# Kernel tuning notes

Measured on AMD Instinct MI355X. Metric: run time of the kernel, lower is better.

Reference implementation:

```python
import jax, jax.numpy as jnp
import numpy as np
from jax import lax


def _causal_depthwise_conv(x, conv_w, conv_b):
    # x: [B, L, D]; conv_w: [D, 1, K]; conv_b: [D]
    K = conv_w.shape[-1]
    xc = jnp.transpose(x, (0, 2, 1))                      # [B, D, L]
    xc = jnp.pad(xc, ((0, 0), (0, 0), (K - 1, 0)))        # left (causal) pad
    D = xc.shape[1]
    y = lax.conv_general_dilated(
        xc, conv_w, window_strides=(1,), padding='VALID',
        dimension_numbers=('NCH', 'OIH', 'NCH'), feature_group_count=D)
    y = y + conv_b[None, :, None]
    return jnp.transpose(y, (0, 2, 1))                    # [B, L, D]


def setup_inputs() -> dict:
    key = jax.random.key(0)
    ks = jax.random.split(key, 7)
    B, L, Dm, S, K = 4, 4096, 2048, 512, 4
    s = 0.02
    x = jax.random.normal(ks[0], (B, L, Dm), dtype=jnp.float32)
    Wxproj = jax.random.normal(ks[1], (2 * S + 1, Dm), dtype=jnp.float32) * s
    Winproj = jax.random.normal(ks[2], (S, Dm), dtype=jnp.float32) * s
    Woutproj = jax.random.normal(ks[3], (Dm, S), dtype=jnp.float32) * s
    conv_w = jax.random.normal(ks[4], (Dm, 1, K), dtype=jnp.float32) * 0.5
    conv_b = jax.random.normal(ks[5], (Dm,), dtype=jnp.float32) * 0.02
    A_log = jnp.log(jnp.arange(1, S + 1, dtype=jnp.float32))
    D = jnp.ones((Dm,), dtype=jnp.float32)
    return {"x": x, "Wxproj": Wxproj, "Winproj": Winproj, "Woutproj": Woutproj,
            "conv_w": conv_w, "conv_b": conv_b, "A_log": A_log, "D": D}


def reference(x, Wxproj, Winproj, Woutproj, conv_w, conv_b, A_log, D):
    S = A_log.shape[0]
    # causal depthwise conv (Conv1d with padding=K-1, truncated to seq_len)
    x_conv = _causal_depthwise_conv(x, conv_w, conv_b)     # [B, L, Dm]
    # SSM parameters from raw x (matches original: x_proj applied to x, not x_conv)
    ssm_params = jnp.einsum('bld,pd->blp', x, Wxproj)      # [B, L, 2S+1]
    Bmat = ssm_params[..., :S]
    Cmat = ssm_params[..., S:2 * S]
    delta = jax.nn.softplus(ssm_params[..., 2 * S:])       # [B, L, 1]
    A = -jnp.exp(A_log)                                    # [S]
    deltaA = jnp.exp(A[None, None, :] * delta)             # [B, L, S]
    x_state = jnp.einsum('bld,sd->bls', x_conv, Winproj)   # [B, L, S]
    Bu = delta * Bmat * x_state                            # [B, L, S]
    # h_t = deltaA_t * h_{t-1} + Bu_t  via associative scan
    def combine(c1, c2):
        a1, b1 = c1
        a2, b2 = c2
        return a1 * a2, a2 * b1 + b2
    _, h = lax.associative_scan(combine, (deltaA, Bu), axis=1)  # [B, L, S]
    h_mod = Cmat * h
    out = jnp.einsum('bls,ds->bld', h_mod, Woutproj) + D[None, None, :] * x_conv
    return out
```

## Files before the change

kernel.cpp:

```cpp
#include <hip/hip_runtime.h>
#include <math.h>

typedef __bf16 bf16_t;
typedef __bf16 bf16x8 __attribute__((ext_vector_type(8)));
typedef __bf16 bf16x4 __attribute__((ext_vector_type(4)));
typedef float  f32x4  __attribute__((ext_vector_type(4)));
typedef float  f32x16 __attribute__((ext_vector_type(16)));

constexpr int Bb  = 4;
constexpr int L   = 4096;
constexpr int Dm  = 2048;
constexpr int S   = 512;
constexpr int M   = Bb * L;
constexpr int NP  = 2 * S + 1;
constexpr int PST = 1024;
constexpr int CL  = 128;
constexpr int NCH = L / CL;
constexpr int TL  = 32;
constexpr int NTC = L / TL;

#define AS1 __attribute__((address_space(1)))
#define AS3 __attribute__((address_space(3)))

__global__ __launch_bounds__(256)
void f2b_kernel(const float* __restrict__ in, bf16_t* __restrict__ out,
                long out8, long in_elems)
{
    long i = (long)blockIdx.x * 256 + threadIdx.x;
    if (i >= out8) return;
    long e = i * 8;
    bf16x8 o;
    if (e + 8 <= in_elems) {
        float4 v0 = *(const float4*)(in + e);
        float4 v1 = *(const float4*)(in + e + 4);
        o[0] = (bf16_t)v0.x; o[1] = (bf16_t)v0.y;
        o[2] = (bf16_t)v0.z; o[3] = (bf16_t)v0.w;
        o[4] = (bf16_t)v1.x; o[5] = (bf16_t)v1.y;
        o[6] = (bf16_t)v1.z; o[7] = (bf16_t)v1.w;
    } else {
        #pragma unroll
        for (int k = 0; k < 8; ++k)
            o[k] = (e + k < in_elems) ? (bf16_t)in[e + k] : (bf16_t)0.f;
    }
    *(bf16x8*)(out + e) = o;
}

__global__ __launch_bounds__(256)
void conv_fused8(const float* __restrict__ x, const float* __restrict__ w,
                 const float* __restrict__ bias,
                 bf16_t* __restrict__ xcb, bf16_t* __restrict__ xb)
{
    const float4* x4 = (const float4*)x;
    int g    = blockIdx.x * 256 + threadIdx.x;
    int d8   = g & 255;
    int rest = g >> 8;
    int c    = rest & (NTC - 1);
    int b    = rest >> 7;
    int d    = d8 * 8;

    float wv[8][4];
    #pragma unroll
    for (int j = 0; j < 8; ++j)
        *(float4*)wv[j] = *(const float4*)&w[(d + j) * 4];
    float bsv[8];
    *(float4*)&bsv[0] = *(const float4*)&bias[d];
    *(float4*)&bsv[4] = *(const float4*)&bias[d + 4];

    const int l0 = c * TL;
    const size_t rowbase = (size_t)b * L;

    float win[3][8];
    #pragma unroll
    for (int i = 0; i < 3; ++i) {
        int lp = l0 - 3 + i;
        if (lp >= 0) {
            size_t rb4 = (rowbase + lp) * 512 + d8 * 2;
            *(float4*)&win[i][0] = x4[rb4];
            *(float4*)&win[i][4] = x4[rb4 + 1];
        } else {
            #pragma unroll
            for (int j = 0; j < 8; ++j) win[i][j] = 0.f;
        }
    }

    for (int t = 0; t < TL; ++t) {
        size_t m = rowbase + l0 + t;
        size_t rb4 = m * 512 + d8 * 2;
        float cur[8];
        *(float4*)&cur[0] = x4[rb4];
        *(float4*)&cur[4] = x4[rb4 + 1];

        bf16x8 oc, ox;
        #pragma unroll
        for (int j = 0; j < 8; ++j) {
            float a = bsv[j];
            a = fmaf(win[0][j], wv[j][0], a);
            a = fmaf(win[1][j], wv[j][1], a);
            a = fmaf(win[2][j], wv[j][2], a);
            a = fmaf(cur[j],    wv[j][3], a);
            oc[j] = (bf16_t)a;
            ox[j] = (bf16_t)cur[j];
        }
        *(bf16x8*)(xcb + m * Dm + d) = oc;
        *(bf16x8*)(xb  + m * Dm + d) = ox;

        #pragma unroll
        for (int j = 0; j < 8; ++j) {
            win[0][j] = win[1][j]; win[1][j] = win[2][j]; win[2][j] = cur[j];
        }
    }
}

__global__ __launch_bounds__(256)
void gemv_delta(const bf16_t* __restrict__ x_bf, const bf16_t* __restrict__ wdt,
                float* __restrict__ delta)
{
    int m    = blockIdx.x * 4 + (threadIdx.x >> 6);
    int lane = threadIdx.x & 63;
    const bf16x8* xr = (const bf16x8*)(x_bf + (size_t)m * Dm);
    const bf16x8* wr = (const bf16x8*)wdt;
    float s = 0.f;
    #pragma unroll
    for (int i = 0; i < 4; ++i) {
        bf16x8 a = xr[i * 64 + lane];
        bf16x8 b = wr[i * 64 + lane];
        #pragma unroll
        for (int j = 0; j < 8; ++j) s += (float)a[j] * (float)b[j];
    }
    #pragma unroll
    for (int off = 32; off >= 1; off >>= 1) s += __shfl_xor(s, off, 64);
    if (lane == 0) {
        delta[m] = (s > 20.f) ? s : log1pf(__expf(s));
    }
}

__device__ __forceinline__ void stage_slabA(const bf16_t* __restrict__ A,
    bf16_t* lds, int ldsbase, int row0, int K, int kcol, int mh,
    int wid, int lrow, int cswz)
{
    #pragma unroll
    for (int round = 0; round < 2; ++round) {
        int Rb = round * 128 + mh * 64 + wid * 8;
        const bf16_t* src = A + (size_t)(row0 + Rb + lrow) * K + kcol + cswz;
        __builtin_amdgcn_global_load_lds(
            (AS1 void*)src, (AS3 void*)(lds + ldsbase + Rb * 64), 16, 0, 0);
    }
}

__device__ __forceinline__ void stage_slabA128(const bf16_t* __restrict__ A,
    bf16_t* lds, int ldsbase, int row0, int K, int kcol,
    int wid, int lrow, int cswz)
{
    #pragma unroll
    for (int round = 0; round < 2; ++round) {
        int Rb = round * 64 + wid * 8;
        const bf16_t* src = A + (size_t)(row0 + Rb + lrow) * K + kcol + cswz;
        __builtin_amdgcn_global_load_lds(
            (AS1 void*)src, (AS3 void*)(lds + ldsbase + Rb * 64), 16, 0, 0);
    }
}

__device__ __forceinline__ void stage_slabB(const bf16_t* __restrict__ B,
    bf16_t* lds, int ldsbase, int col0, int K, int kcol, int nh,
    int wid, int lrow, int cswz)
{
    #pragma unroll
    for (int round = 0; round < 2; ++round) {
        int c  = round * 8 + wid;
        int Rb = (c >> 2) * 64 + nh * 32 + (c & 3) * 8;
        const bf16_t* src = B + (size_t)(col0 + Rb + lrow) * K + kcol + cswz;
        __builtin_amdgcn_global_load_lds(
            (AS1 void*)src, (AS3 void*)(lds + ldsbase + Rb * 64), 16, 0, 0);
    }
}

template <int MH>
__device__ __forceinline__ void load_fragsA32(const bf16_t* lds, int Abase,
    int wm, int l31, int kh, bf16x8 (&af)[2][4])
{
    #pragma unroll
    for (int mi2 = 0; mi2 < 2; ++mi2) {
        const int R = wm * 128 + (MH * 2 + mi2) * 32 + l31;
        #pragma unroll
        for (int ks = 0; ks < 4; ++ks)
            af[mi2][ks] = *(const bf16x8*)(lds + Abase + R * 64 +
                            ((ks * 16 + kh * 8) ^ ((R & 7) << 3)));
    }
}

template <int MI>
__device__ __forceinline__ void load_fragsA32h(const bf16_t* lds, int Abase,
    int wm, int l31, int kh, bf16x8 (&af)[4])
{
    const int R = wm * 64 + MI * 32 + l31;
    #pragma unroll
    for (int ks = 0; ks < 4; ++ks)
        af[ks] = *(const bf16x8*)(lds + Abase + R * 64 +
                    ((ks * 16 + kh * 8) ^ ((R & 7) << 3)));
}

template <int NH>
__device__ __forceinline__ void load_fragsB32(const bf16_t* lds, int Bbase,
    int wn, int l31, int kh, bf16x8 (&bfr)[4])
{
    const int R = wn * 64 + NH * 32 + l31;
    #pragma unroll
    for (int ks = 0; ks < 4; ++ks)
        bfr[ks] = *(const bf16x8*)(lds + Bbase + R * 64 +
                    ((ks * 16 + kh * 8) ^ ((R & 7) << 3)));
}

template <int MH, int NH>
__device__ __forceinline__ void do_mfma32(bf16x8 (&af)[2][4], bf16x8 (&bfr)[4],
                                          f32x16 (&acc)[4][2])
{
    __builtin_amdgcn_s_setprio(1);
    #pragma unroll
    for (int ks = 0; ks < 4; ++ks)
        #pragma unroll
        for (int mi2 = 0; mi2 < 2; ++mi2)
            acc[MH * 2 + mi2][NH] = __builtin_amdgcn_mfma_f32_32x32x16_bf16(
                af[mi2][ks], bfr[ks], acc[MH * 2 + mi2][NH], 0, 0, 0);
    __builtin_amdgcn_s_setprio(0);
}

template <int MI, int NJ>
__device__ __forceinline__ void do_mfma32h(bf16x8 (&af)[4], bf16x8 (&bfr)[4],
                                           f32x16 (&acc)[2][2])
{
    __builtin_amdgcn_s_setprio(1);
    #pragma unroll
    for (int ks = 0; ks < 4; ++ks)
        acc[MI][NJ] = __builtin_amdgcn_mfma_f32_32x32x16_bf16(
            af[ks], bfr[ks], acc[MI][NJ], 0, 0, 0);
    __builtin_amdgcn_s_setprio(0);
}

#define WAITBAR(N) do { \
    asm volatile("s_waitcnt vmcnt(" #N ")" ::: "memory"); \
    __builtin_amdgcn_s_barrier(); } while (0)

template <int EPI>
__global__ __launch_bounds__(512, 2)
void gemm8p(const bf16_t* __restrict__ A, const bf16_t* __restrict__ B,
            int N, int K, int NT,
            bf16_t* __restrict__ Cb, float* __restrict__ Cf,
            const float* __restrict__ e0, const bf16_t* __restrict__ eb)
{
    extern __shared__ __align__(16) char smem_raw[];
    bf16_t* lds = (bf16_t*)smem_raw;

    const int tid  = threadIdx.x;
    const int lane = tid & 63;
    const int wid  = tid >> 6;
    const int wm   = wid >> 2;
    const int wn   = wid & 3;
    const int l31  = lane & 31;
    const int kh   = lane >> 5;
    const int row0 = blockIdx.x * 256;
    const int col0 = blockIdx.y * 256;
    const int lrow = lane >> 3;
    const int cswz = 8 * ((lane & 7) ^ lrow);

    f32x16 acc[4][2];
    #pragma unroll
    for (int i = 0; i < 4; ++i)
        #pragma unroll
        for (int j = 0; j < 2; ++j)
            #pragma unroll
            for (int g = 0; g < 16; ++g) acc[i][j][g] = 0.f;

    stage_slabA(A, lds, 0,     row0, K, 0, 0, wid, lrow, cswz);
    stage_slabB(B, lds, 16384, col0, K, 0, 0, wid, lrow, cswz);
    stage_slabB(B, lds, 16384, col0, K, 0, 1, wid, lrow, cswz);
    stage_slabA(A, lds, 0,     row0, K, 0, 1, wid, lrow, cswz);

    for (int kt = 0; kt < NT; ++kt) {
        const int cur = kt & 1, nxt = cur ^ 1;
        const int Abase = cur * 32768, Bbase = cur * 32768 + 16384;
        const int An = nxt * 32768,   Bn = nxt * 32768 + 16384;
        const int kc = (kt + 1 < NT ? kt + 1 : kt) * 64;

        bf16x8 af[2][4], bfr[4];

        WAITBAR(4);
        load_fragsA32<0>(lds, Abase, wm, l31, kh, af);
        load_fragsB32<0>(lds, Bbase, wn, l31, kh, bfr);
        stage_slabA(A, lds, An, row0, K, kc, 0, wid, lrow, cswz);
        do_mfma32<0, 0>(af, bfr, acc);

        WAITBAR(4);
        load_fragsB32<1>(lds, Bbase, wn, l31, kh, bfr);
        stage_slabB(B, lds, Bn, col0, K, kc, 0, wid, lrow, cswz);
        do_mfma32<0, 1>(af, bfr, acc);

        WAITBAR(4);
        load_fragsA32<1>(lds, Abase, wm, l31, kh, af);
        stage_slabB(B, lds, Bn, col0, K, kc, 1, wid, lrow, cswz);
        do_mfma32<1, 1>(af, bfr, acc);

        load_fragsB32<0>(lds, Bbase, wn, l31, kh, bfr);
        stage_slabA(A, lds, An, row0, K, kc, 1, wid, lrow, cswz);
        do_mfma32<1, 0>(af, bfr, acc);
    }

    #pragma unroll
    for (int mi = 0; mi < 4; ++mi) {
        #pragma unroll
        for (int nj = 0; nj < 2; ++nj) {
            #pragma unroll
            for (int rg = 0; rg < 16; ++rg) {
                int mr = row0 + wm * 128 + mi * 32 + (rg & 3) + 8 * (rg >> 2) + 4 * kh;
                int nc = col0 + wn * 64 + nj * 32 + l31;
                float v = acc[mi][nj][rg];
                if (EPI == 0) {
                    Cb[(size_t)mr * PST + nc] = (bf16_t)v;
                } else {
                    float xc = (float)eb[(size_t)mr * N + nc];
                    Cf[(size_t)mr * N + nc] = v + e0[nc] * xc;
                }
            }
        }
    }
}

__global__ __launch_bounds__(512, 2)
void gemm8ph(const bf16_t* __restrict__ A, const bf16_t* __restrict__ B,
             int N, int K, int NT,
             float* __restrict__ Cf,
             const float* __restrict__ e0, const bf16_t* __restrict__ eb)
{
    extern __shared__ __align__(16) char smem_raw[];
    bf16_t* lds = (bf16_t*)smem_raw;

    const int tid  = threadIdx.x;
    const int lane = tid & 63;
    const int wid  = tid >> 6;
    const int wm   = wid >> 2;
    const int wn   = wid & 3;
    const int l31  = lane & 31;
    const int kh   = lane >> 5;
    const int row0 = blockIdx.x * 128;
    const int col0 = blockIdx.y * 256;
    const int lrow = lane >> 3;
    const int cswz = 8 * ((lane & 7) ^ lrow);

    f32x16 acc[2][2];
    #pragma unroll
    for (int i = 0; i < 2; ++i)
        #pragma unroll
        for (int j = 0; j < 2; ++j)
            #pragma unroll
            for (int g = 0; g < 16; ++g) acc[i][j][g] = 0.f;

    stage_slabA128(A, lds, 0,    row0, K, 0, wid, lrow, cswz);
    stage_slabB(B, lds, 8192, col0, K, 0, 0, wid, lrow, cswz);
    stage_slabB(B, lds, 8192, col0, K, 0, 1, wid, lrow, cswz);

    for (int kt = 0; kt < NT; ++kt) {
        const int cur = kt & 1, nxt = cur ^ 1;
        const int Abase = cur * 24576, Bbase = cur * 24576 + 8192;
        const int An = nxt * 24576,   Bn = nxt * 24576 + 8192;
        const int kc = (kt + 1 < NT ? kt + 1 : kt) * 64;

        bf16x8 af[4], bfr[4];

        WAITBAR(2);
        load_fragsA32h<0>(lds, Abase, wm, l31, kh, af);
        load_fragsB32<0>(lds, Bbase, wn, l31, kh, bfr);
        stage_slabA128(A, lds, An, row0, K, kc, wid, lrow, cswz);
        do_mfma32h<0, 0>(af, bfr, acc);

        WAITBAR(2);
        load_fragsB32<1>(lds, Bbase, wn, l31, kh, bfr);
        stage_slabB(B, lds, Bn, col0, K, kc, 0, wid, lrow, cswz);
        do_mfma32h<0, 1>(af, bfr, acc);

        load_fragsA32h<1>(lds, Abase, wm, l31, kh, af);
        stage_slabB(B, lds, Bn, col0, K, kc, 1, wid, lrow, cswz);
        do_mfma32h<1, 1>(af, bfr, acc);

        load_fragsB32<0>(lds, Bbase, wn, l31, kh, bfr);
        do_mfma32h<1, 0>(af, bfr, acc);
    }

    #pragma unroll
    for (int mi = 0; mi < 2; ++mi) {
        #pragma unroll
        for (int nj = 0; nj < 2; ++nj) {
            #pragma unroll
            for (int rg = 0; rg < 16; ++rg) {
                int mr = row0 + wm * 64 + mi * 32 + (rg & 3) + 8 * (rg >> 2) + 4 * kh;
                int nc = col0 + wn * 64 + nj * 32 + l31;
                float Bm = (float)eb[(size_t)mr * PST + nc];
                Cf[(size_t)mr * N + nc] = e0[mr] * Bm * acc[mi][nj][rg];
            }
        }
    }
}

__global__ __launch_bounds__(256)
void scan_pass1(const float* __restrict__ Bu, const float* __restrict__ delta,
                const float* __restrict__ A_log,
                float* __restrict__ cP, float* __restrict__ cH)
{
    int s = blockIdx.x * 256 + threadIdx.x;
    int c = blockIdx.y;
    int b = blockIdx.z;
    float Acoef = -expf(A_log[s]);
    float P = 1.f, h = 0.f;
    int mbase = b * L + c * CL;
    for (int t = 0; t < CL; ++t) {
        float a = __expf(Acoef * delta[mbase + t]);
        float u = Bu[(size_t)(mbase + t) * S + s];
        h = fmaf(a, h, u);
        P *= a;
    }
    int id = b * S + s;
    cP[(size_t)id * NCH + c] = P;
    cH[(size_t)id * NCH + c] = h;
}

__global__ __launch_bounds__(256)
void scan_pass2(const float* __restrict__ cP, const float* __restrict__ cH,
                float* __restrict__ init)
{
    int id = blockIdx.x * 256 + threadIdx.x;
    if (id < Bb * S) {
        float h = 0.f;
        for (int c = 0; c < NCH; ++c) {
            init[(size_t)id * NCH + c] = h;
            h = fmaf(cP[(size_t)id * NCH + c], h, cH[(size_t)id * NCH + c]);
        }
    }
}

__global__ __launch_bounds__(256)
void scan_pass3(const float* __restrict__ Bu, const float* __restrict__ delta,
                const bf16_t* __restrict__ params_bf,
                const float* __restrict__ A_log,
                const float* __restrict__ init, bf16_t* __restrict__ hmod)
{
    int s = blockIdx.x * 256 + threadIdx.x;
    int c = blockIdx.y;
    int b = blockIdx.z;
    float Acoef = -expf(A_log[s]);
    float h = init[(size_t)(b * S + s) * NCH + c];
    int mbase = b * L + c * CL;
    for (int t = 0; t < CL; ++t) {
        int m = mbase + t;
        float a = __expf(Acoef * delta[m]);
        float u = Bu[(size_t)m * S + s];
        h = fmaf(a, h, u);
        float Cm = (float)params_bf[(size_t)m * PST + S + s];
        hmod[(size_t)m * S + s] = (bf16_t)(Cm * h);
    }
}

extern "C" void kernel_launch(void* const* d_in, const int* in_sizes, int n_in,
                              void* d_out, int out_size, void* d_ws, size_t ws_size,
                              hipStream_t stream)
{
    const float* x        = (const float*)d_in[0];
    const float* Wxproj   = (const float*)d_in[1];
    const float* Winproj  = (const float*)d_in[2];
    const float* Woutproj = (const float*)d_in[3];
    const float* conv_w   = (const float*)d_in[4];
    const float* conv_b   = (const float*)d_in[5];
    const float* A_log    = (const float*)d_in[6];
    const float* Dvec     = (const float*)d_in[7];
    float* out = (float*)d_out;

    float* ws_Bu    = (float*)d_ws;
    float* ws_delta = ws_Bu + (size_t)M * S;
    float* ws_cP    = ws_delta + M;
    float* ws_cH    = ws_cP + (size_t)Bb * S * NCH;
    float* ws_init  = ws_cH + (size_t)Bb * S * NCH;
    bf16_t* params_bf = (bf16_t*)(ws_init + (size_t)Bb * S * NCH);
    bf16_t* x_bf      = params_bf + (size_t)M * PST;
    bf16_t* hmod_bf   = x_bf;
    bf16_t* xconv_bf  = x_bf + (size_t)M * Dm;
    bf16_t* Wx_bf     = xconv_bf + (size_t)M * Dm;
    bf16_t* Win_bf    = Wx_bf + (size_t)NP * Dm;
    bf16_t* Wout_bf   = Win_bf + (size_t)S * Dm;

    hipFuncSetAttribute((const void*)gemm8p<0>,
                        hipFuncAttributeMaxDynamicSharedMemorySize, 131072);
    hipFuncSetAttribute((const void*)gemm8p<2>,
                        hipFuncAttributeMaxDynamicSharedMemorySize, 131072);
    hipFuncSetAttribute((const void*)gemm8ph,
                        hipFuncAttributeMaxDynamicSharedMemorySize, 98304);

    long wx8 = (long)NP * Dm / 8;
    f2b_kernel<<<(wx8 + 255) / 256, 256, 0, stream>>>(Wxproj, Wx_bf, wx8, (long)NP * Dm);
    long wi8 = (long)S * Dm / 8;
    f2b_kernel<<<(wi8 + 255) / 256, 256, 0, stream>>>(Winproj, Win_bf, wi8, (long)S * Dm);
    f2b_kernel<<<(wi8 + 255) / 256, 256, 0, stream>>>(Woutproj, Wout_bf, wi8, (long)Dm * S);

    conv_fused8<<<(Bb * NTC * 256) / 256, 256, 0, stream>>>(
        x, conv_w, conv_b, xconv_bf, x_bf);

    dim3 g1(M / 256, PST / 256);
    gemm8p<0><<<g1, 512, 131072, stream>>>(x_bf, Wx_bf, PST, Dm, Dm / 64,
                                           params_bf, nullptr, nullptr, nullptr);

    gemv_delta<<<M / 4, 256, 0, stream>>>(x_bf, Wx_bf + (size_t)PST * Dm, ws_delta);

    dim3 g2(M / 128, S / 256);
    gemm8ph<<<g2, 512, 98304, stream>>>(xconv_bf, Win_bf, S, Dm, Dm / 64,
                                        ws_Bu, ws_delta, params_bf);

    dim3 gs(S / 256, NCH, Bb);
    scan_pass1<<<gs, 256, 0, stream>>>(ws_Bu, ws_delta, A_log, ws_cP, ws_cH);
    scan_pass2<<<(Bb * S) / 256, 256, 0, stream>>>(ws_cP, ws_cH, ws_init);
    scan_pass3<<<gs, 256, 0, stream>>>(ws_Bu, ws_delta, params_bf, A_log,
                                       ws_init, hmod_bf);

    dim3 g3(M / 256, Dm / 256);
    gemm8p<2><<<g3, 512, 131072, stream>>>(hmod_bf, Wout_bf, Dm, S, S / 64,
                                           nullptr, out, Dvec, xconv_bf);
}
```

Measured before the change: 293.5 us.

## Fuse delta GEMV into conv, store Bu in bf16, shrink scan chunks

```diff
diff --git a/kernel.cpp b/kernel.cpp
--- a/kernel.cpp
+++ b/kernel.cpp
@@ -14,9 +14,9 @@
 constexpr int M   = Bb * L;
 constexpr int NP  = 2 * S + 1;
 constexpr int PST = 1024;
-constexpr int CL  = 128;
+constexpr int CL  = 32;
 constexpr int NCH = L / CL;
-constexpr int TL  = 32;
+constexpr int TL  = 8;
 constexpr int NTC = L / TL;
 
 #define AS1 __attribute__((address_space(1)))
@@ -46,91 +46,91 @@
 }
 
 __global__ __launch_bounds__(256)
-void conv_fused8(const float* __restrict__ x, const float* __restrict__ w,
-                 const float* __restrict__ bias,
-                 bf16_t* __restrict__ xcb, bf16_t* __restrict__ xb)
-{
-    const float4* x4 = (const float4*)x;
+void conv_bf8(const bf16_t* __restrict__ xb, const float* __restrict__ w,
+              const float* __restrict__ bias, const float* __restrict__ wdt,
+              bf16_t* __restrict__ xcb, float* __restrict__ dpart)
+{
     int g    = blockIdx.x * 256 + threadIdx.x;
     int d8   = g & 255;
     int rest = g >> 8;
     int c    = rest & (NTC - 1);
-    int b    = rest >> 7;
+    int b    = rest >> 9;
     int d    = d8 * 8;
-
-    float wv[8][4];
+    int wv   = threadIdx.x >> 6;
+    int lane = threadIdx.x & 63;
+
+    float wv8[8][4];
     #pragma unroll
     for (int j = 0; j < 8; ++j)
-        *(float4*)wv[j] = *(const float4*)&w[(d + j) * 4];
-    float bsv[8];
-    *(float4*)&bsv[0] = *(const float4*)&bias[d];
-    *(float4*)&bsv[4] = *(const float4*)&bias[d + 4];
+        *(float4*)wv8[j] = *(const float4*)&w[(d + j) * 4];
+    float bias8[8];
+    *(float4*)&bias8[0] = *(const float4*)&bias[d];
+    *(float4*)&bias8[4] = *(const float4*)&bias[d + 4];
+    float wdt8[8];
+    *(float4*)&wdt8[0] = *(const float4*)&wdt[d];
+    *(float4*)&wdt8[4] = *(const float4*)&wdt[d + 4];
 
     const int l0 = c * TL;
     const size_t rowbase = (size_t)b * L;
 
-    float win[3][8];
+    bf16x8 win[3];
     #pragma unroll
     for (int i = 0; i < 3; ++i) {
         int lp = l0 - 3 + i;
         if (lp >= 0) {
-            size_t rb4 = (rowbase + lp) * 512 + d8 * 2;
-            *(float4*)&win[i][0] = x4[rb4];
-            *(float4*)&win[i][4] = x4[rb4 + 1];
+            win[i] = *(const bf16x8*)(xb + (rowbase + lp) * Dm + d);
         } else {
             #pragma unroll
-            for (int j = 0; j < 8; ++j) win[i][j] = 0.f;
+            for (int j = 0; j < 8; ++j) win[i][j] = (bf16_t)0.f;
         }
     }
 
+    float pd[TL];
+    #pragma unroll
     for (int t = 0; t < TL; ++t) {
-        size_t m = rowbase + l0 + t;
-        size_t rb4 = m * 512 + d8 * 2;
-        float cur[8];
-        *(float4*)&cur[0] = x4[rb4];
-        *(float4*)&cur[4] = x4[rb4 + 1];
-
-        bf16x8 oc, ox;
+        size_t ri = (rowbase + l0 + t) * Dm + d;
+        bf16x8 cur = *(const bf16x8*)(xb + ri);
+        bf16x8 oc;
+        float p = 0.f;
         #pragma unroll
         for (int j = 0; j < 8; ++j) {
-            float a = bsv[j];
-            a = fmaf(win[0][j], wv[j][0], a);
-            a = fmaf(win[1][j], wv[j][1], a);
-            a = fmaf(win[2][j], wv[j][2], a);
-            a = fmaf(cur[j],    wv[j][3], a);
+            float cj = (float)cur[j];
+            float a = bias8[j];
+            a = fmaf((float)win[0][j], wv8[j][0], a);
+            a = fmaf((float)win[1][j], wv8[j][1], a);
+            a = fmaf((float)win[2][j], wv8[j][2], a);
+            a = fmaf(cj,               wv8[j][3], a);
             oc[j] = (bf16_t)a;
-            ox[j] = (bf16_t)cur[j];
+            p = fmaf(cj, wdt8[j], p);
         }
-        *(bf16x8*)(xcb + m * Dm + d) = oc;
-        *(bf16x8*)(xb  + m * Dm + d) = ox;
-
-        #pragma unroll
-        for (int j = 0; j < 8; ++j) {
-            win[0][j] = win[1][j]; win[1][j] = win[2][j]; win[2][j] = cur[j];
-        }
+        *(bf16x8*)(xcb + ri) = oc;
+        pd[t] = p;
+        win[0] = win[1]; win[1] = win[2]; win[2] = cur;
+    }
+
+    #pragma unroll
+    for (int t = 0; t < TL; ++t) {
+        float s = pd[t];
+        #pragma unroll
+        for (int off = 32; off >= 1; off >>= 1) s += __shfl_xor(s, off, 64);
+        pd[t] = s;
+    }
+    if (lane == 0) {
+        int mbase = b * L + l0;
+        #pragma unroll
+        for (int t = 0; t < TL; ++t)
+            dpart[(size_t)(mbase + t) * 4 + wv] = pd[t];
     }
 }
 
 __global__ __launch_bounds__(256)
-void gemv_delta(const bf16_t* __restrict__ x_bf, const bf16_t* __restrict__ wdt,
-                float* __restrict__ delta)
-{
-    int m    = blockIdx.x * 4 + (threadIdx.x >> 6);
-    int lane = threadIdx.x & 63;
-    const bf16x8* xr = (const bf16x8*)(x_bf + (size_t)m * Dm);
-    const bf16x8* wr = (const bf16x8*)wdt;
-    float s = 0.f;
-    #pragma unroll
-    for (int i = 0; i < 4; ++i) {
-        bf16x8 a = xr[i * 64 + lane];
-        bf16x8 b = wr[i * 64 + lane];
-        #pragma unroll
-        for (int j = 0; j < 8; ++j) s += (float)a[j] * (float)b[j];
-    }
-    #pragma unroll
-    for (int off = 32; off >= 1; off >>= 1) s += __shfl_xor(s, off, 64);
-    if (lane == 0) {
-        delta[m] = (s > 20.f) ? s : log1pf(__expf(s));
+void delta_reduce(const float* __restrict__ dpart, float* __restrict__ delta)
+{
+    int i = blockIdx.x * 256 + threadIdx.x;
+    if (i < M) {
+        float4 p = *(const float4*)(dpart + (size_t)i * 4);
+        float z = (p.x + p.y) + (p.z + p.w);
+        delta[i] = (z > 20.f) ? z : log1pf(__expf(z));
     }
 }
 
@@ -327,7 +327,7 @@
 __global__ __launch_bounds__(512, 2)
 void gemm8ph(const bf16_t* __restrict__ A, const bf16_t* __restrict__ B,
              int N, int K, int NT,
-             float* __restrict__ Cf,
+             bf16_t* __restrict__ Bub,
              const float* __restrict__ e0, const bf16_t* __restrict__ eb)
 {
     extern __shared__ __align__(16) char smem_raw[];
@@ -393,14 +393,14 @@
                 int mr = row0 + wm * 64 + mi * 32 + (rg & 3) + 8 * (rg >> 2) + 4 * kh;
                 int nc = col0 + wn * 64 + nj * 32 + l31;
                 float Bm = (float)eb[(size_t)mr * PST + nc];
-                Cf[(size_t)mr * N + nc] = e0[mr] * Bm * acc[mi][nj][rg];
+                Bub[(size_t)mr * N + nc] = (bf16_t)(e0[mr] * Bm * acc[mi][nj][rg]);
             }
         }
     }
 }
 
 __global__ __launch_bounds__(256)
-void scan_pass1(const float* __restrict__ Bu, const float* __restrict__ delta,
+void scan_pass1(const bf16_t* __restrict__ Bu, const float* __restrict__ delta,
                 const float* __restrict__ A_log,
                 float* __restrict__ cP, float* __restrict__ cH)
 {
@@ -412,7 +412,7 @@
     int mbase = b * L + c * CL;
     for (int t = 0; t < CL; ++t) {
         float a = __expf(Acoef * delta[mbase + t]);
-        float u = Bu[(size_t)(mbase + t) * S + s];
+        float u = (float)Bu[(size_t)(mbase + t) * S + s];
         h = fmaf(a, h, u);
         P *= a;
     }
@@ -436,7 +436,7 @@
 }
 
 __global__ __launch_bounds__(256)
-void scan_pass3(const float* __restrict__ Bu, const float* __restrict__ delta,
+void scan_pass3(const bf16_t* __restrict__ Bu, const float* __restrict__ delta,
                 const bf16_t* __restrict__ params_bf,
                 const float* __restrict__ A_log,
                 const float* __restrict__ init, bf16_t* __restrict__ hmod)
@@ -450,7 +450,7 @@
     for (int t = 0; t < CL; ++t) {
         int m = mbase + t;
         float a = __expf(Acoef * delta[m]);
-        float u = Bu[(size_t)m * S + s];
+        float u = (float)Bu[(size_t)m * S + s];
         h = fmaf(a, h, u);
         float Cm = (float)params_bf[(size_t)m * PST + S + s];
         hmod[(size_t)m * S + s] = (bf16_t)(Cm * h);
@@ -471,17 +471,18 @@
     const float* Dvec     = (const float*)d_in[7];
     float* out = (float*)d_out;
 
-    float* ws_Bu    = (float*)d_ws;
-    float* ws_delta = ws_Bu + (size_t)M * S;
-    float* ws_cP    = ws_delta + M;
+    float* ws_delta = (float*)d_ws;
+    float* ws_dpart = ws_delta + M;
+    float* ws_cP    = ws_dpart + (size_t)M * 4;
     float* ws_cH    = ws_cP + (size_t)Bb * S * NCH;
     float* ws_init  = ws_cH + (size_t)Bb * S * NCH;
-    bf16_t* params_bf = (bf16_t*)(ws_init + (size_t)Bb * S * NCH);
+    bf16_t* Bu_bf     = (bf16_t*)(ws_init + (size_t)Bb * S * NCH);
+    bf16_t* params_bf = Bu_bf + (size_t)M * S;
     bf16_t* x_bf      = params_bf + (size_t)M * PST;
     bf16_t* hmod_bf   = x_bf;
     bf16_t* xconv_bf  = x_bf + (size_t)M * Dm;
     bf16_t* Wx_bf     = xconv_bf + (size_t)M * Dm;
-    bf16_t* Win_bf    = Wx_bf + (size_t)NP * Dm;
+    bf16_t* Win_bf    = Wx_bf + (size_t)PST * Dm;
     bf16_t* Wout_bf   = Win_bf + (size_t)S * Dm;
 
     hipFuncSetAttribute((const void*)gemm8p<0>,
@@ -491,29 +492,32 @@
     hipFuncSetAttribute((const void*)gemm8ph,
                         hipFuncAttributeMaxDynamicSharedMemorySize, 98304);
 
-    long wx8 = (long)NP * Dm / 8;
-    f2b_kernel<<<(wx8 + 255) / 256, 256, 0, stream>>>(Wxproj, Wx_bf, wx8, (long)NP * Dm);
+    long x8 = (long)M * Dm / 8;
+    f2b_kernel<<<(x8 + 255) / 256, 256, 0, stream>>>(x, x_bf, x8, (long)M * Dm);
+
+    long wx8 = (long)PST * Dm / 8;
+    f2b_kernel<<<(wx8 + 255) / 256, 256, 0, stream>>>(Wxproj, Wx_bf, wx8, (long)PST * Dm);
     long wi8 = (long)S * Dm / 8;
     f2b_kernel<<<(wi8 + 255) / 256, 256, 0, stream>>>(Winproj, Win_bf, wi8, (long)S * Dm);
     f2b_kernel<<<(wi8 + 255) / 256, 256, 0, stream>>>(Woutproj, Wout_bf, wi8, (long)Dm * S);
 
-    conv_fused8<<<(Bb * NTC * 256) / 256, 256, 0, stream>>>(
-        x, conv_w, conv_b, xconv_bf, x_bf);
+    conv_bf8<<<Bb * NTC, 256, 0, stream>>>(
+        x_bf, conv_w, conv_b, Wxproj + (size_t)(2 * S) * Dm, xconv_bf, ws_dpart);
+
+    delta_reduce<<<M / 256, 256, 0, stream>>>(ws_dpart, ws_delta);
 
     dim3 g1(M / 256, PST / 256);
     gemm8p<0><<<g1, 512, 131072, stream>>>(x_bf, Wx_bf, PST, Dm, Dm / 64,
                                            params_bf, nullptr, nullptr, nullptr);
 
-    gemv_delta<<<M / 4, 256, 0, stream>>>(x_bf, Wx_bf + (size_t)PST * Dm, ws_delta);
-
     dim3 g2(M / 128, S / 256);
     gemm8ph<<<g2, 512, 98304, stream>>>(xconv_bf, Win_bf, S, Dm, Dm / 64,
-                                        ws_Bu, ws_delta, params_bf);
+                                        Bu_bf, ws_delta, params_bf);
 
     dim3 gs(S / 256, NCH, Bb);
-    scan_pass1<<<gs, 256, 0, stream>>>(ws_Bu, ws_delta, A_log, ws_cP, ws_cH);
+    scan_pass1<<<gs, 256, 0, stream>>>(Bu_bf, ws_delta, A_log, ws_cP, ws_cH);
     scan_pass2<<<(Bb * S) / 256, 256, 0, stream>>>(ws_cP, ws_cH, ws_init);
-    scan_pass3<<<gs, 256, 0, stream>>>(ws_Bu, ws_delta, params_bf, A_log,
+    scan_pass3<<<gs, 256, 0, stream>>>(Bu_bf, ws_delta, params_bf, A_log,
                                        ws_init, hmod_bf);
 
     dim3 g3(M / 256, Dm / 256);
```

Result: faster. 277.6 us (-5.4%).
